# Optimization experiments

Measured on AMD Instinct MI355X. Metric: run time of the kernel, lower is better.

Reference implementation:

```python
import jax, jax.numpy as jnp
import numpy as np

N = 500000
V = 50000
GF = 64
OC = 256

def _lin(key, din, dout):
    k1, k2 = jax.random.split(key)
    w = jax.random.normal(k1, (din, dout), dtype=jnp.float32) * 0.02
    b = jax.random.normal(k2, (dout,), dtype=jnp.float32) * 0.02
    return w, b

def setup_inputs() -> dict:
    key = jax.random.key(0)
    ks = jax.random.split(key, 12)
    inp_feat = jax.random.normal(ks[0], (N, 6), dtype=jnp.float32)
    vox2point_idx = jax.random.randint(ks[1], (N,), 0, V, dtype=jnp.int32)
    w1x, b1x = _lin(ks[2], 3, GF)
    w2x, b2x = _lin(ks[3], GF, OC // 8)
    w1r, b1r = _lin(ks[4], 3, GF)
    w2r, b2r = _lin(ks[5], GF, OC // 8)
    wax, bax = _lin(ks[6], OC // 4, OC // 8)
    war, bar = _lin(ks[7], OC // 4, OC // 8)
    wv1, bv1 = _lin(ks[8], OC // 2, OC // 2)
    w3, b3 = _lin(ks[9], OC, OC)
    w4, b4 = _lin(ks[10], OC, OC)
    wv2, bv2 = _lin(ks[11], OC, OC)
    return dict(inp_feat=inp_feat, vox2point_idx=vox2point_idx, num_vox=V,
                w1x=w1x, b1x=b1x, w2x=w2x, b2x=b2x,
                w1r=w1r, b1r=b1r, w2r=w2r, b2r=b2r,
                wax=wax, bax=bax, war=war, bar=bar,
                wv1=wv1, bv1=bv1, w3=w3, b3=b3, w4=w4, b4=b4,
                wv2=wv2, bv2=bv2)

def reference(inp_feat, vox2point_idx, num_vox,
              w1x, b1x, w2x, b2x, w1r, b1r, w2r, b2r,
              wax, bax, war, bar, wv1, bv1, w3, b3, w4, b4, wv2, bv2):
    relu = jax.nn.relu
    xyz = inp_feat[:, :3]
    rgb = inp_feat[:, 3:]
    fx = relu(relu(xyz @ w1x + b1x) @ w2x + b2x)   # [N, 32]
    fr = relu(relu(rgb @ w1r + b1r) @ w2r + b2r)   # [N, 32]
    comb = jnp.concatenate([fx, fr], axis=-1)       # [N, 64]
    pf2 = jnp.concatenate([
        fx, fx * jax.nn.sigmoid(comb @ wax + bax),
        fr, fr * jax.nn.sigmoid(comb @ war + bar)], axis=-1)  # [N, 128]
    # scatter-max to voxels; torch_scatter fills empty segments with 0 and
    # pf2 >= 0 elementwise, so clamp -inf (jax empty fill) to 0 for parity.
    vox = jax.ops.segment_max(pf2, vox2point_idx, num_segments=num_vox)
    vox = jnp.maximum(vox, 0.0)                     # [V, 128]
    vox = relu(vox @ wv1 + bv1)
    pg = vox[vox2point_idx]                          # gather back [N, 128]
    pf3 = jnp.concatenate([pg, pf2], axis=-1)        # [N, 256]
    pf5 = relu(relu(pf3 @ w3 + b3) @ w4 + b4)        # [N, 256]
    vox2 = jax.ops.segment_max(pf5, vox2point_idx, num_segments=num_vox)
    vox2 = jnp.maximum(vox2, 0.0)
    return relu(vox2 @ wv2 + bv2)                    # [V, 256]
```

## Files before the change

kernel.cpp:

```cpp
#include <hip/hip_runtime.h>

#define NPTS 500000
#define NVOX 50000
#define NBLK 196

typedef unsigned short u16;
typedef unsigned int u32;
typedef __attribute__((ext_vector_type(8))) short short8;
typedef __attribute__((ext_vector_type(4))) float floatx4;
typedef __attribute__((ext_vector_type(4))) unsigned int uintx4;
typedef __attribute__((ext_vector_type(2))) unsigned int uintx2;
typedef __attribute__((ext_vector_type(2))) unsigned short us2;

__device__ __forceinline__ u32 pkbf(float lo, float hi) {
    u32 r;
    asm("v_cvt_pk_bf16_f32 %0, %1, %2" : "=v"(r) : "v"(lo), "v"(hi));
    return r;
}
__device__ __forceinline__ u16 f2bf(float f) {
    u32 r;
    asm("v_cvt_pk_bf16_f32 %0, %1, %1" : "=v"(r) : "v"(f));
    return (u16)r;
}
__device__ __forceinline__ u32 pmax(u32 a, u32 b) {
    us2 r = __builtin_elementwise_max(__builtin_bit_cast(us2, a), __builtin_bit_cast(us2, b));
    return __builtin_bit_cast(u32, r);
}

__global__ void k_wtransform(const float* __restrict__ W, u16* __restrict__ Wf, int K, int N) {
    int t = blockIdx.x * 256 + threadIdx.x;
    if (t >= K * N) return;
    int k = t / N, n = t - k * N;
    int kk = k >> 5, q = (k >> 3) & 3, j = k & 7;
    Wf[((size_t)((kk * 4 + q) * N + n) << 3) + j] = f2bf(W[t]);
}

__global__ void k_wcat(const float* __restrict__ w2x, const float* __restrict__ w2r, u16* __restrict__ wcatf) {
    int t = blockIdx.x * 256 + threadIdx.x;
    if (t >= 128 * 64) return;
    int k = t >> 6, n = t & 63;
    float v;
    if (k < 64) v = (n < 32) ? w2x[k * 32 + n] : 0.f;
    else        v = (n >= 32) ? w2r[(k - 64) * 32 + (n - 32)] : 0.f;
    int kk = k >> 5, q = (k >> 3) & 3, j = k & 7;
    wcatf[((size_t)((kk * 4 + q) * 64 + n) << 3) + j] = f2bf(v);
}

__global__ void k_watt(const float* __restrict__ wax, const float* __restrict__ war, u16* __restrict__ wattf) {
    int t = blockIdx.x * 256 + threadIdx.x;
    if (t >= 64 * 64) return;
    int k = t >> 6, n = t & 63;
    float v = (n < 32) ? wax[k * 32 + n] : war[k * 32 + (n - 32)];
    int kk = k >> 5, q = (k >> 3) & 3, j = k & 7;
    wattf[((size_t)((kk * 4 + q) * 64 + n) << 3) + j] = f2bf(v);
}

__global__ void k_hist(const int* __restrict__ idx, int* __restrict__ hcnt) {
    int i = blockIdx.x * 256 + threadIdx.x;
    if (i < NPTS) atomicAdd(&hcnt[idx[i]], 1);
}

__global__ __launch_bounds__(256) void k_scan1(const int* __restrict__ hcnt, int* __restrict__ bsum) {
    __shared__ int wsum[4];
    int t = threadIdx.x;
    int i = blockIdx.x * 256 + t;
    int c = (i < NVOX) ? hcnt[i] : 0;
    #pragma unroll
    for (int d = 32; d >= 1; d >>= 1) c += __shfl_xor(c, d, 64);
    if ((t & 63) == 0) wsum[t >> 6] = c;
    __syncthreads();
    if (t == 0) bsum[blockIdx.x] = wsum[0] + wsum[1] + wsum[2] + wsum[3];
}

__global__ __launch_bounds__(256) void k_scan2(const int* __restrict__ bsum, int* __restrict__ boff) {
    __shared__ int wsum[4];
    int t = threadIdx.x, lane = t & 63, w = t >> 6;
    int c = (t < NBLK) ? bsum[t] : 0;
    int v = c;
    #pragma unroll
    for (int d = 1; d < 64; d <<= 1) {
        int o = __shfl_up(v, d, 64);
        if (lane >= d) v += o;
    }
    if (lane == 63) wsum[w] = v;
    __syncthreads();
    int wo = 0;
    #pragma unroll
    for (int k = 0; k < 4; k++) if (k < w) wo += wsum[k];
    if (t < NBLK) boff[t] = wo + v - c;
}

__global__ __launch_bounds__(256) void k_scan3(const int* __restrict__ hcnt, const int* __restrict__ boff,
                                               int* __restrict__ cur) {
    __shared__ int wsum[4];
    int t = threadIdx.x, lane = t & 63, w = t >> 6;
    int i = blockIdx.x * 256 + t;
    int c = (i < NVOX) ? hcnt[i] : 0;
    int v = c;
    #pragma unroll
    for (int d = 1; d < 64; d <<= 1) {
        int o = __shfl_up(v, d, 64);
        if (lane >= d) v += o;
    }
    if (lane == 63) wsum[w] = v;
    __syncthreads();
    int wo = 0;
    #pragma unroll
    for (int k = 0; k < 4; k++) if (k < w) wo += wsum[k];
    if (i < NVOX) cur[i] = boff[blockIdx.x] + wo + v - c;
}

__global__ void k_scatter(const int* __restrict__ idx, int* __restrict__ cur,
                          int* __restrict__ sptid, int* __restrict__ svid) {
    int i = blockIdx.x * 256 + threadIdx.x;
    if (i < NPTS) {
        int v = idx[i];
        int pos = atomicAdd(&cur[v], 1);
        sptid[pos] = i;
        svid[pos] = v;
    }
}

__global__ __launch_bounds__(256) void k_pointfeat(
    const float* __restrict__ inp, const int* __restrict__ sptid, const int* __restrict__ svid,
    const float* __restrict__ w1x, const float* __restrict__ b1x,
    const float* __restrict__ w1r, const float* __restrict__ b1r,
    const u16* __restrict__ wcatf, const float* __restrict__ b2x, const float* __restrict__ b2r,
    const u16* __restrict__ wattf, const float* __restrict__ bax, const float* __restrict__ bar,
    u16* __restrict__ pf2s, float* __restrict__ voxmax)
{
    __shared__ u16 hbuf[64 * 136];
    __shared__ u16 cbuf[64 * 72];
    __shared__ float wl[512];
    __shared__ int lvid[64];
    int t = threadIdx.x;
    int i0 = blockIdx.x * 64;
    int mcnt = NPTS - i0; if (mcnt > 64) mcnt = 64;
    for (int s = t; s < 512; s += 256) {
        float v;
        if (s < 192)      v = w1x[s];
        else if (s < 256) v = b1x[s - 192];
        else if (s < 448) v = w1r[s - 256];
        else              v = b1r[s - 448];
        wl[s] = v;
    }
    if (t < 64) lvid[t] = (t < mcnt) ? svid[i0 + t] : -1;
    __syncthreads();
    {
        int m = t >> 2, c = t & 3;
        float x0 = 0, x1 = 0, x2 = 0, r0 = 0, r1 = 0, r2 = 0;
        if (m < mcnt) {
            const float* p = inp + (size_t)sptid[i0 + m] * 6;
            x0 = p[0]; x1 = p[1]; x2 = p[2]; r0 = p[3]; r1 = p[4]; r2 = p[5];
        }
        u16* hb = &hbuf[m * 136 + c * 16];
        #pragma unroll
        for (int jp = 0; jp < 8; jp++) {
            int c0 = c * 16 + 2 * jp, c1 = c0 + 1;
            float hx0 = fmaxf(wl[192 + c0] + x0 * wl[c0] + x1 * wl[64 + c0] + x2 * wl[128 + c0], 0.f);
            float hx1 = fmaxf(wl[192 + c1] + x0 * wl[c1] + x1 * wl[64 + c1] + x2 * wl[128 + c1], 0.f);
            float hr0 = fmaxf(wl[448 + c0] + r0 * wl[256 + c0] + r1 * wl[320 + c0] + r2 * wl[384 + c0], 0.f);
            float hr1 = fmaxf(wl[448 + c1] + r0 * wl[256 + c1] + r1 * wl[320 + c1] + r2 * wl[384 + c1], 0.f);
            *(u32*)(hb + 2 * jp)      = pkbf(hx0, hx1);
            *(u32*)(hb + 64 + 2 * jp) = pkbf(hr0, hr1);
        }
    }
    __syncthreads();
    int wave = t >> 6, l = t & 63, q = l >> 4, lm = l & 15;
    int n = wave * 16 + lm;
    floatx4 acc[4];
    #pragma unroll
    for (int a = 0; a < 4; a++) acc[a] = (floatx4){0.f, 0.f, 0.f, 0.f};
    #pragma unroll
    for (int kk = 0; kk < 4; kk++) {
        short8 bfrag = *(const short8*)&wcatf[(size_t)((kk * 4 + q) * 64 + n) << 3];
        #pragma unroll
        for (int tm = 0; tm < 4; tm++) {
            short8 afrag = *(const short8*)&hbuf[(tm * 16 + lm) * 136 + kk * 32 + q * 8];
            acc[tm] = __builtin_amdgcn_mfma_f32_16x16x32_bf16(afrag, bfrag, acc[tm], 0, 0, 0);
        }
    }
    float bv = (n < 32) ? b2x[n] : b2r[n - 32];
    float comb_keep[4][4];
    #pragma unroll
    for (int tm = 0; tm < 4; tm++)
        #pragma unroll
        for (int r = 0; r < 4; r++) {
            float v = fmaxf(acc[tm][r] + bv, 0.f);
            comb_keep[tm][r] = v;
            int m = tm * 16 + q * 4 + r;
            cbuf[m * 72 + n] = f2bf(v);
        }
    __syncthreads();
    floatx4 acc2[4];
    #pragma unroll
    for (int a = 0; a < 4; a++) acc2[a] = (floatx4){0.f, 0.f, 0.f, 0.f};
    #pragma unroll
    for (int kk = 0; kk < 2; kk++) {
        short8 bfrag = *(const short8*)&wattf[(size_t)((kk * 4 + q) * 64 + n) << 3];
        #pragma unroll
        for (int tm = 0; tm < 4; tm++) {
            short8 afrag = *(const short8*)&cbuf[(tm * 16 + lm) * 72 + kk * 32 + q * 8];
            acc2[tm] = __builtin_amdgcn_mfma_f32_16x16x32_bf16(afrag, bfrag, acc2[tm], 0, 0, 0);
        }
    }
    float bv2 = (n < 32) ? bax[n] : bar[n - 32];
    int pp = (n < 32) ? n : 32 + n;
    #pragma unroll
    for (int tm = 0; tm < 4; tm++)
        #pragma unroll
        for (int r = 0; r < 4; r++) {
            float att = acc2[tm][r] + bv2;
            float sg = 1.f / (1.f + __expf(-att));
            float plain = comb_keep[tm][r];
            float gated = plain * sg;
            int m = tm * 16 + q * 4 + r;
            hbuf[m * 136 + pp] = f2bf(plain);
            hbuf[m * 136 + pp + 32] = f2bf(gated);
        }
    __syncthreads();
    {
        int row = t >> 2, seg = t & 3;
        if (row < mcnt) {
            const u16* src = &hbuf[row * 136 + seg * 32];
            u16* dst = pf2s + (size_t)(i0 + row) * 128 + seg * 32;
            *(uintx4*)dst = *(const uintx4*)src;
            *(uintx4*)(dst + 8) = *(const uintx4*)(src + 8);
        }
    }
    {
        int c2 = t & 63;
        int h = t >> 6;
        int r0 = h * 16;
        int r1 = r0 + 16; if (r1 > mcnt) r1 = mcnt;
        u32 mm = 0;
        int pvid = -1;
        for (int r = r0; r < r1; r++) {
            int vid = lvid[r];
            if (vid != pvid) {
                if (pvid >= 0) {
                    int* addr = (int*)(voxmax + (size_t)pvid * 128 + 2 * c2);
                    if (mm << 16) atomicMax(addr, (int)(mm << 16));
                    if (mm & 0xffff0000u) atomicMax(addr + 1, (int)(mm & 0xffff0000u));
                }
                pvid = vid; mm = 0;
            }
            u32 u = *(const u32*)&hbuf[r * 136 + 2 * c2];
            mm = pmax(mm, u);
        }
        if (pvid >= 0) {
            int* addr = (int*)(voxmax + (size_t)pvid * 128 + 2 * c2);
            if (mm << 16) atomicMax(addr, (int)(mm << 16));
            if (mm & 0xffff0000u) atomicMax(addr + 1, (int)(mm & 0xffff0000u));
        }
    }
}

template<int K, int N, bool ABF16, bool OUT_BF16>
__global__ __launch_bounds__(256) void k_gemm_relu(
    const void* __restrict__ Ap, const u16* __restrict__ Wf,
    const float* __restrict__ bias, void* __restrict__ outp, int M)
{
    constexpr int STRIDE = K + 8;
    constexpr int TN = N / 64;
    constexpr int KSTEPS = K / 32;
    constexpr int CW = K / 4;
    __shared__ u16 lds[64 * STRIDE];
    int i0 = blockIdx.x * 64;
    int mcnt = M - i0; if (mcnt > 64) mcnt = 64;
    int t = threadIdx.x;
    {
        int row = t >> 2, cseg = t & 3;
        u16* dst = &lds[row * STRIDE + cseg * CW];
        if (row < mcnt) {
            if (ABF16) {
                const u16* src = (const u16*)Ap + (size_t)(i0 + row) * K + cseg * CW;
                #pragma unroll
                for (int c = 0; c < CW / 8; c++)
                    *(uintx4*)(dst + c * 8) = *(const uintx4*)(src + c * 8);
            } else {
                const float* src = (const float*)Ap + (size_t)(i0 + row) * K + cseg * CW;
                #pragma unroll
                for (int c = 0; c < CW / 8; c++) {
                    float4 v0 = *(const float4*)(src + c * 8);
                    float4 v1 = *(const float4*)(src + c * 8 + 4);
                    uintx4 rr = (uintx4){ pkbf(v0.x, v0.y), pkbf(v0.z, v0.w),
                                          pkbf(v1.x, v1.y), pkbf(v1.z, v1.w) };
                    *(uintx4*)(dst + c * 8) = rr;
                }
            }
        } else {
            short8 z = {0, 0, 0, 0, 0, 0, 0, 0};
            #pragma unroll
            for (int c = 0; c < CW / 8; c++) *(short8*)(dst + c * 8) = z;
        }
    }
    __syncthreads();
    int wave = t >> 6, l = t & 63;
    int q = l >> 4, lm = l & 15;
    int wn0 = wave * (N / 4);
    floatx4 acc[4][TN];
    #pragma unroll
    for (int a = 0; a < 4; a++)
        #pragma unroll
        for (int b = 0; b < TN; b++) acc[a][b] = (floatx4){0.f, 0.f, 0.f, 0.f};
    #pragma unroll
    for (int kk = 0; kk < KSTEPS; kk++) {
        short8 afrag[4], bfrag[TN];
        #pragma unroll
        for (int tm = 0; tm < 4; tm++)
            afrag[tm] = *(const short8*)&lds[(tm * 16 + lm) * STRIDE + kk * 32 + q * 8];
        #pragma unroll
        for (int tn = 0; tn < TN; tn++)
            bfrag[tn] = *(const short8*)&Wf[(size_t)((kk * 4 + q) * N + wn0 + tn * 16 + lm) * 8];
        #pragma unroll
        for (int tm = 0; tm < 4; tm++)
            #pragma unroll
            for (int tn = 0; tn < TN; tn++)
                acc[tm][tn] = __builtin_amdgcn_mfma_f32_16x16x32_bf16(afrag[tm], bfrag[tn], acc[tm][tn], 0, 0, 0);
    }
    #pragma unroll
    for (int tm = 0; tm < 4; tm++)
        #pragma unroll
        for (int tn = 0; tn < TN; tn++) {
            int n = wn0 + tn * 16 + lm;
            float bv = bias[n];
            #pragma unroll
            for (int r = 0; r < 4; r++) {
                int m = tm * 16 + q * 4 + r;
                if (m < mcnt) {
                    float v = fmaxf(acc[tm][tn][r] + bv, 0.f);
                    if (OUT_BF16) ((u16*)outp)[(size_t)(i0 + m) * N + n] = f2bf(v);
                    else          ((float*)outp)[(size_t)(i0 + m) * N + n] = v;
                }
            }
        }
}

__global__ __launch_bounds__(512) void k_pointmlp(
    const u16* __restrict__ voxf, const u16* __restrict__ pf2s, const int* __restrict__ svid,
    const u16* __restrict__ w3f, const float* __restrict__ b3,
    const u16* __restrict__ w4f, const float* __restrict__ b4,
    float* __restrict__ vox2)
{
    constexpr int STRIDE = 264;
    __shared__ u16 lds[64 * STRIDE];
    __shared__ int lvid[64];
    __shared__ float bl[512];
    int i0 = blockIdx.x * 64;
    int mcnt = NPTS - i0; if (mcnt > 64) mcnt = 64;
    int t = threadIdx.x;
    if (t < 64) lvid[t] = (t < mcnt) ? svid[i0 + t] : -1;
    bl[t] = (t < 256) ? b3[t] : b4[t - 256];
    {
        int row = t >> 3, j = t & 7;
        int sv = (row < mcnt) ? svid[i0 + row] : 0;
        u16* dstb = &lds[row * STRIDE + j * 16];
        uintx4 a0 = (uintx4){0,0,0,0}, a1 = a0, b0 = a0, b1 = a0;
        if (row < mcnt) {
            const u16* s0 = voxf + (size_t)sv * 128 + j * 16;
            const u16* s1 = pf2s + (size_t)(i0 + row) * 128 + j * 16;
            a0 = *(const uintx4*)s0; a1 = *(const uintx4*)(s0 + 8);
            b0 = *(const uintx4*)s1; b1 = *(const uintx4*)(s1 + 8);
        }
        *(uintx4*)(dstb) = a0;
        *(uintx4*)(dstb + 8) = a1;
        *(uintx4*)(dstb + 128) = b0;
        *(uintx4*)(dstb + 136) = b1;
    }
    __syncthreads();
    int wave = t >> 6, l = t & 63;
    int q = l >> 4, lm = l & 15;
    int wm0 = wave * 32;
    floatx4 acc[2][4];
    #pragma unroll
    for (int a = 0; a < 2; a++)
        #pragma unroll
        for (int b = 0; b < 4; b++) acc[a][b] = (floatx4){0.f, 0.f, 0.f, 0.f};
    #pragma unroll
    for (int kk = 0; kk < 8; kk++) {
        short8 wfrag[2], bfrag[4];
        #pragma unroll
        for (int tm = 0; tm < 2; tm++)
            wfrag[tm] = *(const short8*)&w3f[(size_t)((kk * 4 + q) * 256 + wm0 + tm * 16 + lm) * 8];
        #pragma unroll
        for (int tn = 0; tn < 4; tn++)
            bfrag[tn] = *(const short8*)&lds[(tn * 16 + lm) * STRIDE + kk * 32 + q * 8];
        #pragma unroll
        for (int tm = 0; tm < 2; tm++)
            #pragma unroll
            for (int tn = 0; tn < 4; tn++)
                acc[tm][tn] = __builtin_amdgcn_mfma_f32_16x16x32_bf16(wfrag[tm], bfrag[tn], acc[tm][tn], 0, 0, 0);
    }
    __syncthreads();
    #pragma unroll
    for (int tm = 0; tm < 2; tm++) {
        float4 bq = *(const float4*)&bl[wm0 + tm * 16 + 4 * q];
        #pragma unroll
        for (int tn = 0; tn < 4; tn++) {
            u32 lo = pkbf(fmaxf(acc[tm][tn][0] + bq.x, 0.f), fmaxf(acc[tm][tn][1] + bq.y, 0.f));
            u32 hi = pkbf(fmaxf(acc[tm][tn][2] + bq.z, 0.f), fmaxf(acc[tm][tn][3] + bq.w, 0.f));
            *(uintx2*)&lds[(tn * 16 + lm) * STRIDE + wm0 + tm * 16 + 4 * q] = (uintx2){lo, hi};
        }
    }
    __syncthreads();
    floatx4 acc2[2][4];
    #pragma unroll
    for (int a = 0; a < 2; a++)
        #pragma unroll
        for (int b = 0; b < 4; b++) acc2[a][b] = (floatx4){0.f, 0.f, 0.f, 0.f};
    #pragma unroll
    for (int kk = 0; kk < 8; kk++) {
        short8 wfrag[2], bfrag[4];
        #pragma unroll
        for (int tm = 0; tm < 2; tm++)
            wfrag[tm] = *(const short8*)&w4f[(size_t)((kk * 4 + q) * 256 + wm0 + tm * 16 + lm) * 8];
        #pragma unroll
        for (int tn = 0; tn < 4; tn++)
            bfrag[tn] = *(const short8*)&lds[(tn * 16 + lm) * STRIDE + kk * 32 + q * 8];
        #pragma unroll
        for (int tm = 0; tm < 2; tm++)
            #pragma unroll
            for (int tn = 0; tn < 4; tn++)
                acc2[tm][tn] = __builtin_amdgcn_mfma_f32_16x16x32_bf16(wfrag[tm], bfrag[tn], acc2[tm][tn], 0, 0, 0);
    }
    __syncthreads();
    #pragma unroll
    for (int tm = 0; tm < 2; tm++) {
        float4 bq = *(const float4*)&bl[256 + wm0 + tm * 16 + 4 * q];
        #pragma unroll
        for (int tn = 0; tn < 4; tn++) {
            u32 lo = pkbf(fmaxf(acc2[tm][tn][0] + bq.x, 0.f), fmaxf(acc2[tm][tn][1] + bq.y, 0.f));
            u32 hi = pkbf(fmaxf(acc2[tm][tn][2] + bq.z, 0.f), fmaxf(acc2[tm][tn][3] + bq.w, 0.f));
            *(uintx2*)&lds[(tn * 16 + lm) * STRIDE + wm0 + tm * 16 + 4 * q] = (uintx2){lo, hi};
        }
    }
    __syncthreads();
    {
        int c2 = t & 127;
        int h = t >> 7;
        int r0 = h * 16;
        int r1 = r0 + 16; if (r1 > mcnt) r1 = mcnt;
        u32 mm = 0;
        int pvid = -1;
        for (int r = r0; r < r1; r++) {
            int vid = lvid[r];
            if (vid != pvid) {
                if (pvid >= 0) {
                    int* addr = (int*)(vox2 + (size_t)pvid * 256 + 2 * c2);
                    if (mm << 16) atomicMax(addr, (int)(mm << 16));
                    if (mm & 0xffff0000u) atomicMax(addr + 1, (int)(mm & 0xffff0000u));
                }
                pvid = vid; mm = 0;
            }
            u32 u = *(const u32*)&lds[r * STRIDE + 2 * c2];
            mm = pmax(mm, u);
        }
        if (pvid >= 0) {
            int* addr = (int*)(vox2 + (size_t)pvid * 256 + 2 * c2);
            if (mm << 16) atomicMax(addr, (int)(mm << 16));
            if (mm & 0xffff0000u) atomicMax(addr + 1, (int)(mm & 0xffff0000u));
        }
    }
}

extern "C" void kernel_launch(void* const* d_in, const int* in_sizes, int n_in,
                              void* d_out, int out_size, void* d_ws, size_t ws_size,
                              hipStream_t stream) {
    const float* inp = (const float*)d_in[0];
    const int*   idx = (const int*)d_in[1];
    const float* w1x = (const float*)d_in[3];  const float* b1x = (const float*)d_in[4];
    const float* w2x = (const float*)d_in[5];  const float* b2x = (const float*)d_in[6];
    const float* w1r = (const float*)d_in[7];  const float* b1r = (const float*)d_in[8];
    const float* w2r = (const float*)d_in[9];  const float* b2r = (const float*)d_in[10];
    const float* wax = (const float*)d_in[11]; const float* bax = (const float*)d_in[12];
    const float* war = (const float*)d_in[13]; const float* bar = (const float*)d_in[14];
    const float* wv1 = (const float*)d_in[15]; const float* bv1 = (const float*)d_in[16];
    const float* w3  = (const float*)d_in[17]; const float* b3  = (const float*)d_in[18];
    const float* w4  = (const float*)d_in[19]; const float* b4  = (const float*)d_in[20];
    const float* wv2 = (const float*)d_in[21]; const float* bv2 = (const float*)d_in[22];
    float* out = (float*)d_out;

    char* ws = (char*)d_ws;
    u16*   pf2s   = (u16*)ws;   ws += (size_t)NPTS * 128 * sizeof(u16);
    float* voxmax = (float*)ws; ws += (size_t)NVOX * 128 * sizeof(float);
    u16*   voxf   = (u16*)ws;   ws += (size_t)NVOX * 128 * sizeof(u16);
    float* vox2   = (float*)ws; ws += (size_t)NVOX * 256 * sizeof(float);
    u16*   w3f    = (u16*)ws;   ws += 65536 * sizeof(u16);
    u16*   w4f    = (u16*)ws;   ws += 65536 * sizeof(u16);
    u16*   wv1f   = (u16*)ws;   ws += 16384 * sizeof(u16);
    u16*   wv2f   = (u16*)ws;   ws += 65536 * sizeof(u16);
    u16*   wcatf  = (u16*)ws;   ws += 8192 * sizeof(u16);
    u16*   wattf  = (u16*)ws;   ws += 4096 * sizeof(u16);
    int*   hcnt   = (int*)ws;   ws += (size_t)NVOX * sizeof(int);
    int*   cur    = (int*)ws;   ws += (size_t)NVOX * sizeof(int);
    int*   bsum   = (int*)ws;   ws += (size_t)NBLK * sizeof(int);
    int*   boff   = (int*)ws;   ws += (size_t)NBLK * sizeof(int);
    int*   sptid  = (int*)ws;   ws += (size_t)NPTS * sizeof(int);
    int*   svid   = (int*)ws;   ws += (size_t)NPTS * sizeof(int);

    hipMemsetAsync(hcnt, 0, (size_t)NVOX * sizeof(int), stream);
    hipMemsetAsync(voxmax, 0, (size_t)NVOX * 128 * sizeof(float), stream);
    hipMemsetAsync(vox2, 0, (size_t)NVOX * 256 * sizeof(float), stream);

    k_wtransform<<<256, 256, 0, stream>>>(w3, w3f, 256, 256);
    k_wtransform<<<256, 256, 0, stream>>>(w4, w4f, 256, 256);
    k_wtransform<<<64,  256, 0, stream>>>(wv1, wv1f, 128, 128);
    k_wtransform<<<256, 256, 0, stream>>>(wv2, wv2f, 256, 256);
    k_wcat<<<32, 256, 0, stream>>>(w2x, w2r, wcatf);
    k_watt<<<16, 256, 0, stream>>>(wax, war, wattf);

    k_hist<<<(NPTS + 255) / 256, 256, 0, stream>>>(idx, hcnt);
    k_scan1<<<NBLK, 256, 0, stream>>>(hcnt, bsum);
    k_scan2<<<1, 256, 0, stream>>>(bsum, boff);
    k_scan3<<<NBLK, 256, 0, stream>>>(hcnt, boff, cur);
    k_scatter<<<(NPTS + 255) / 256, 256, 0, stream>>>(idx, cur, sptid, svid);

    k_pointfeat<<<(NPTS + 63) / 64, 256, 0, stream>>>(
        inp, sptid, svid, w1x, b1x, w1r, b1r, wcatf, b2x, b2r, wattf, bax, bar, pf2s, voxmax);

    k_gemm_relu<128, 128, false, true><<<(NVOX + 63) / 64, 256, 0, stream>>>(
        (const void*)voxmax, wv1f, bv1, (void*)voxf, NVOX);

    k_pointmlp<<<(NPTS + 63) / 64, 512, 0, stream>>>(
        voxf, pf2s, svid, w3f, b3, w4f, b4, vox2);

    k_gemm_relu<256, 256, false, false><<<(NVOX + 63) / 64, 256, 0, stream>>>(
        (const void*)vox2, wv2f, bv2, (void*)out, NVOX);
}
```

Before: 494.8 us.

## Hoist voxel half of first point GEMM to per-voxel precompute

The first half of the pf3@w3 product (the gathered voxel features times the top half of w3, plus b3) depends only on the voxel. It is now computed once per voxel in a new fused k_voxmlp kernel that chains the wv1 layer with this partial product. The point kernel then runs only K=128 for the first GEMM and adds a gathered fp32 vox3 row before the ReLU. This removes half of the layer-1 MFMA work over 500k points, at the cost of gathering 1KB fp32 rows per point instead of 256B bf16 rows and a larger workspace buffer.

```diff
diff --git a/kernel.cpp b/kernel.cpp
--- a/kernel.cpp
+++ b/kernel.cpp
@@ -252,6 +252,107 @@
             int* addr = (int*)(voxmax + (size_t)pvid * 128 + 2 * c2);
             if (mm << 16) atomicMax(addr, (int)(mm << 16));
             if (mm & 0xffff0000u) atomicMax(addr + 1, (int)(mm & 0xffff0000u));
+        }
+    }
+}
+
+__global__ __launch_bounds__(256) void k_voxmlp(
+    const float* __restrict__ voxmax, const u16* __restrict__ wv1f, const float* __restrict__ bv1,
+    const u16* __restrict__ w3f, const float* __restrict__ b3, float* __restrict__ vox3)
+{
+    constexpr int STRIDE = 136;
+    __shared__ u16 lds[64 * STRIDE];
+    __shared__ float bl[384];
+    int i0 = blockIdx.x * 64;
+    int mcnt = NVOX - i0; if (mcnt > 64) mcnt = 64;
+    int t = threadIdx.x;
+    for (int s = t; s < 384; s += 256) bl[s] = (s < 128) ? bv1[s] : b3[s - 128];
+    {
+        int row = t >> 2, cseg = t & 3;
+        u16* dst = &lds[row * STRIDE + cseg * 32];
+        if (row < mcnt) {
+            const float* src = voxmax + (size_t)(i0 + row) * 128 + cseg * 32;
+            #pragma unroll
+            for (int c = 0; c < 4; c++) {
+                float4 v0 = *(const float4*)(src + c * 8);
+                float4 v1 = *(const float4*)(src + c * 8 + 4);
+                uintx4 rr = (uintx4){ pkbf(v0.x, v0.y), pkbf(v0.z, v0.w),
+                                      pkbf(v1.x, v1.y), pkbf(v1.z, v1.w) };
+                *(uintx4*)(dst + c * 8) = rr;
+            }
+        } else {
+            uintx4 z = {0, 0, 0, 0};
+            #pragma unroll
+            for (int c = 0; c < 4; c++) *(uintx4*)(dst + c * 8) = z;
+        }
+    }
+    __syncthreads();
+    int wave = t >> 6, l = t & 63, q = l >> 4, lm = l & 15;
+    int wm1 = wave * 32;
+    floatx4 a1[2][4];
+    #pragma unroll
+    for (int a = 0; a < 2; a++)
+        #pragma unroll
+        for (int b = 0; b < 4; b++) a1[a][b] = (floatx4){0.f, 0.f, 0.f, 0.f};
+    #pragma unroll
+    for (int kk = 0; kk < 4; kk++) {
+        short8 wfrag[2], bfrag[4];
+        #pragma unroll
+        for (int tm = 0; tm < 2; tm++)
+            wfrag[tm] = *(const short8*)&wv1f[(size_t)((kk * 4 + q) * 128 + wm1 + tm * 16 + lm) * 8];
+        #pragma unroll
+        for (int tn = 0; tn < 4; tn++)
+            bfrag[tn] = *(const short8*)&lds[(tn * 16 + lm) * STRIDE + kk * 32 + q * 8];
+        #pragma unroll
+        for (int tm = 0; tm < 2; tm++)
+            #pragma unroll
+            for (int tn = 0; tn < 4; tn++)
+                a1[tm][tn] = __builtin_amdgcn_mfma_f32_16x16x32_bf16(wfrag[tm], bfrag[tn], a1[tm][tn], 0, 0, 0);
+    }
+    __syncthreads();
+    #pragma unroll
+    for (int tm = 0; tm < 2; tm++) {
+        float4 bq = *(const float4*)&bl[wm1 + tm * 16 + 4 * q];
+        #pragma unroll
+        for (int tn = 0; tn < 4; tn++) {
+            u32 lo = pkbf(fmaxf(a1[tm][tn][0] + bq.x, 0.f), fmaxf(a1[tm][tn][1] + bq.y, 0.f));
+            u32 hi = pkbf(fmaxf(a1[tm][tn][2] + bq.z, 0.f), fmaxf(a1[tm][tn][3] + bq.w, 0.f));
+            *(uintx2*)&lds[(tn * 16 + lm) * STRIDE + wm1 + tm * 16 + 4 * q] = (uintx2){lo, hi};
+        }
+    }
+    __syncthreads();
+    int wm0 = wave * 64;
+    floatx4 a2[4][4];
+    #pragma unroll
+    for (int a = 0; a < 4; a++)
+        #pragma unroll
+        for (int b = 0; b < 4; b++) a2[a][b] = (floatx4){0.f, 0.f, 0.f, 0.f};
+    #pragma unroll
+    for (int kk = 0; kk < 4; kk++) {
+        short8 wfrag[4], bfrag[4];
+        #pragma unroll
+        for (int tm = 0; tm < 4; tm++)
+            wfrag[tm] = *(const short8*)&w3f[(size_t)((kk * 4 + q) * 256 + wm0 + tm * 16 + lm) * 8];
+        #pragma unroll
+        for (int tn = 0; tn < 4; tn++)
+            bfrag[tn] = *(const short8*)&lds[(tn * 16 + lm) * STRIDE + kk * 32 + q * 8];
+        #pragma unroll
+        for (int tm = 0; tm < 4; tm++)
+            #pragma unroll
+            for (int tn = 0; tn < 4; tn++)
+                a2[tm][tn] = __builtin_amdgcn_mfma_f32_16x16x32_bf16(wfrag[tm], bfrag[tn], a2[tm][tn], 0, 0, 0);
+    }
+    #pragma unroll
+    for (int tm = 0; tm < 4; tm++) {
+        float4 bq = *(const float4*)&bl[128 + wm0 + tm * 16 + 4 * q];
+        #pragma unroll
+        for (int tn = 0; tn < 4; tn++) {
+            int row = tn * 16 + lm;
+            if (row < mcnt) {
+                floatx4 o = { a2[tm][tn][0] + bq.x, a2[tm][tn][1] + bq.y,
+                              a2[tm][tn][2] + bq.z, a2[tm][tn][3] + bq.w };
+                *(floatx4*)&vox3[(size_t)(i0 + row) * 256 + wm0 + tm * 16 + 4 * q] = o;
+            }
         }
     }
 }
@@ -338,35 +439,29 @@
 }
 
 __global__ __launch_bounds__(512) void k_pointmlp(
-    const u16* __restrict__ voxf, const u16* __restrict__ pf2s, const int* __restrict__ svid,
-    const u16* __restrict__ w3f, const float* __restrict__ b3,
-    const u16* __restrict__ w4f, const float* __restrict__ b4,
+    const float* __restrict__ vox3, const u16* __restrict__ pf2s, const int* __restrict__ svid,
+    const u16* __restrict__ w3f, const u16* __restrict__ w4f, const float* __restrict__ b4,
     float* __restrict__ vox2)
 {
     constexpr int STRIDE = 264;
     __shared__ u16 lds[64 * STRIDE];
     __shared__ int lvid[64];
-    __shared__ float bl[512];
+    __shared__ float bl[256];
     int i0 = blockIdx.x * 64;
     int mcnt = NPTS - i0; if (mcnt > 64) mcnt = 64;
     int t = threadIdx.x;
     if (t < 64) lvid[t] = (t < mcnt) ? svid[i0 + t] : -1;
-    bl[t] = (t < 256) ? b3[t] : b4[t - 256];
+    if (t < 256) bl[t] = b4[t];
     {
         int row = t >> 3, j = t & 7;
-        int sv = (row < mcnt) ? svid[i0 + row] : 0;
         u16* dstb = &lds[row * STRIDE + j * 16];
-        uintx4 a0 = (uintx4){0,0,0,0}, a1 = a0, b0 = a0, b1 = a0;
+        uintx4 b0 = (uintx4){0, 0, 0, 0}, b1 = b0;
         if (row < mcnt) {
-            const u16* s0 = voxf + (size_t)sv * 128 + j * 16;
             const u16* s1 = pf2s + (size_t)(i0 + row) * 128 + j * 16;
-            a0 = *(const uintx4*)s0; a1 = *(const uintx4*)(s0 + 8);
             b0 = *(const uintx4*)s1; b1 = *(const uintx4*)(s1 + 8);
         }
-        *(uintx4*)(dstb) = a0;
-        *(uintx4*)(dstb + 8) = a1;
-        *(uintx4*)(dstb + 128) = b0;
-        *(uintx4*)(dstb + 136) = b1;
+        *(uintx4*)(dstb) = b0;
+        *(uintx4*)(dstb + 8) = b1;
     }
     __syncthreads();
     int wave = t >> 6, l = t & 63;
@@ -378,11 +473,52 @@
         #pragma unroll
         for (int b = 0; b < 4; b++) acc[a][b] = (floatx4){0.f, 0.f, 0.f, 0.f};
     #pragma unroll
+    for (int kk = 0; kk < 4; kk++) {
+        short8 wfrag[2], bfrag[4];
+        #pragma unroll
+        for (int tm = 0; tm < 2; tm++)
+            wfrag[tm] = *(const short8*)&w3f[(size_t)(((kk + 4) * 4 + q) * 256 + wm0 + tm * 16 + lm) * 8];
+        #pragma unroll
+        for (int tn = 0; tn < 4; tn++)
+            bfrag[tn] = *(const short8*)&lds[(tn * 16 + lm) * STRIDE + kk * 32 + q * 8];
+        #pragma unroll
+        for (int tm = 0; tm < 2; tm++)
+            #pragma unroll
+            for (int tn = 0; tn < 4; tn++)
+                acc[tm][tn] = __builtin_amdgcn_mfma_f32_16x16x32_bf16(wfrag[tm], bfrag[tn], acc[tm][tn], 0, 0, 0);
+    }
+    floatx4 vx[2][4];
+    #pragma unroll
+    for (int tn = 0; tn < 4; tn++) {
+        int vid = lvid[tn * 16 + lm];
+        #pragma unroll
+        for (int tm = 0; tm < 2; tm++) {
+            if (vid >= 0) vx[tm][tn] = *(const floatx4*)&vox3[(size_t)vid * 256 + wm0 + tm * 16 + 4 * q];
+            else          vx[tm][tn] = (floatx4){0.f, 0.f, 0.f, 0.f};
+        }
+    }
+    __syncthreads();
+    #pragma unroll
+    for (int tm = 0; tm < 2; tm++) {
+        #pragma unroll
+        for (int tn = 0; tn < 4; tn++) {
+            u32 lo = pkbf(fmaxf(acc[tm][tn][0] + vx[tm][tn][0], 0.f), fmaxf(acc[tm][tn][1] + vx[tm][tn][1], 0.f));
+            u32 hi = pkbf(fmaxf(acc[tm][tn][2] + vx[tm][tn][2], 0.f), fmaxf(acc[tm][tn][3] + vx[tm][tn][3], 0.f));
+            *(uintx2*)&lds[(tn * 16 + lm) * STRIDE + wm0 + tm * 16 + 4 * q] = (uintx2){lo, hi};
+        }
+    }
+    __syncthreads();
+    floatx4 acc2[2][4];
+    #pragma unroll
+    for (int a = 0; a < 2; a++)
+        #pragma unroll
+        for (int b = 0; b < 4; b++) acc2[a][b] = (floatx4){0.f, 0.f, 0.f, 0.f};
+    #pragma unroll
     for (int kk = 0; kk < 8; kk++) {
         short8 wfrag[2], bfrag[4];
         #pragma unroll
         for (int tm = 0; tm < 2; tm++)
-            wfrag[tm] = *(const short8*)&w3f[(size_t)((kk * 4 + q) * 256 + wm0 + tm * 16 + lm) * 8];
+            wfrag[tm] = *(const short8*)&w4f[(size_t)((kk * 4 + q) * 256 + wm0 + tm * 16 + lm) * 8];
         #pragma unroll
         for (int tn = 0; tn < 4; tn++)
             bfrag[tn] = *(const short8*)&lds[(tn * 16 + lm) * STRIDE + kk * 32 + q * 8];
@@ -390,44 +526,12 @@
         for (int tm = 0; tm < 2; tm++)
             #pragma unroll
             for (int tn = 0; tn < 4; tn++)
-                acc[tm][tn] = __builtin_amdgcn_mfma_f32_16x16x32_bf16(wfrag[tm], bfrag[tn], acc[tm][tn], 0, 0, 0);
+                acc2[tm][tn] = __builtin_amdgcn_mfma_f32_16x16x32_bf16(wfrag[tm], bfrag[tn], acc2[tm][tn], 0, 0, 0);
     }
     __syncthreads();
     #pragma unroll
     for (int tm = 0; tm < 2; tm++) {
         float4 bq = *(const float4*)&bl[wm0 + tm * 16 + 4 * q];
-        #pragma unroll
-        for (int tn = 0; tn < 4; tn++) {
-            u32 lo = pkbf(fmaxf(acc[tm][tn][0] + bq.x, 0.f), fmaxf(acc[tm][tn][1] + bq.y, 0.f));
-            u32 hi = pkbf(fmaxf(acc[tm][tn][2] + bq.z, 0.f), fmaxf(acc[tm][tn][3] + bq.w, 0.f));
-            *(uintx2*)&lds[(tn * 16 + lm) * STRIDE + wm0 + tm * 16 + 4 * q] = (uintx2){lo, hi};
-        }
-    }
-    __syncthreads();
-    floatx4 acc2[2][4];
-    #pragma unroll
-    for (int a = 0; a < 2; a++)
-        #pragma unroll
-        for (int b = 0; b < 4; b++) acc2[a][b] = (floatx4){0.f, 0.f, 0.f, 0.f};
-    #pragma unroll
-    for (int kk = 0; kk < 8; kk++) {
-        short8 wfrag[2], bfrag[4];
-        #pragma unroll
-        for (int tm = 0; tm < 2; tm++)
-            wfrag[tm] = *(const short8*)&w4f[(size_t)((kk * 4 + q) * 256 + wm0 + tm * 16 + lm) * 8];
-        #pragma unroll
-        for (int tn = 0; tn < 4; tn++)
-            bfrag[tn] = *(const short8*)&lds[(tn * 16 + lm) * STRIDE + kk * 32 + q * 8];
-        #pragma unroll
-        for (int tm = 0; tm < 2; tm++)
-            #pragma unroll
-            for (int tn = 0; tn < 4; tn++)
-                acc2[tm][tn] = __builtin_amdgcn_mfma_f32_16x16x32_bf16(wfrag[tm], bfrag[tn], acc2[tm][tn], 0, 0, 0);
-    }
-    __syncthreads();
-    #pragma unroll
-    for (int tm = 0; tm < 2; tm++) {
-        float4 bq = *(const float4*)&bl[256 + wm0 + tm * 16 + 4 * q];
         #pragma unroll
         for (int tn = 0; tn < 4; tn++) {
             u32 lo = pkbf(fmaxf(acc2[tm][tn][0] + bq.x, 0.f), fmaxf(acc2[tm][tn][1] + bq.y, 0.f));
@@ -484,7 +588,7 @@
     char* ws = (char*)d_ws;
     u16*   pf2s   = (u16*)ws;   ws += (size_t)NPTS * 128 * sizeof(u16);
     float* voxmax = (float*)ws; ws += (size_t)NVOX * 128 * sizeof(float);
-    u16*   voxf   = (u16*)ws;   ws += (size_t)NVOX * 128 * sizeof(u16);
+    float* vox3   = (float*)ws; ws += (size_t)NVOX * 256 * sizeof(float);
     float* vox2   = (float*)ws; ws += (size_t)NVOX * 256 * sizeof(float);
     u16*   w3f    = (u16*)ws;   ws += 65536 * sizeof(u16);
     u16*   w4f    = (u16*)ws;   ws += 65536 * sizeof(u16);
@@ -519,11 +623,11 @@
     k_pointfeat<<<(NPTS + 63) / 64, 256, 0, stream>>>(
         inp, sptid, svid, w1x, b1x, w1r, b1r, wcatf, b2x, b2r, wattf, bax, bar, pf2s, voxmax);
 
-    k_gemm_relu<128, 128, false, true><<<(NVOX + 63) / 64, 256, 0, stream>>>(
-        (const void*)voxmax, wv1f, bv1, (void*)voxf, NVOX);
+    k_voxmlp<<<(NVOX + 63) / 64, 256, 0, stream>>>(
+        voxmax, wv1f, bv1, w3f, b3, vox3);
 
     k_pointmlp<<<(NPTS + 63) / 64, 512, 0, stream>>>(
-        voxf, pf2s, svid, w3f, b3, w4f, b4, vox2);
+        vox3, pf2s, svid, w3f, w4f, b4, vox2);
 
     k_gemm_relu<256, 256, false, false><<<(NVOX + 63) / 64, 256, 0, stream>>>(
         (const void*)vox2, wv2f, bv2, (void*)out, NVOX);
```

Result: no change. 498.2 us (+0.7%).
